# Optimization experiments

Hardware: AMD Instinct MI355X
Metric: run time of the kernel (lower is better)

Reference implementation:

```python
import jax, jax.numpy as jnp
import numpy as np

B, S, E, H = 4, 1024, 1024, 16
D = E // H          # head_dim = 64
ROT = 32            # rotary dims (first ROT channels of each head)


def _rope(x, freqs):
    # x: [B, H, S, D]; freqs: [1, 1, S, ROT]
    r = freqs.shape[-1]
    xl, xr = x[..., :r], x[..., r:]
    half = r // 2
    rot = jnp.concatenate([-xl[..., half:], xl[..., :half]], axis=-1)  # rotate_half
    xl = xl * jnp.cos(freqs) + rot * jnp.sin(freqs)
    return jnp.concatenate([xl, xr], axis=-1)


def setup_inputs() -> dict:
    key = jax.random.key(0)
    ks = jax.random.split(key, 7)
    std = 0.02
    return {
        "hidden_states": jax.random.normal(ks[0], (B, S, E), jnp.float32),
        "rotary_pos_emb": jax.random.normal(ks[1], (1, S, ROT), jnp.float32),
        "q_w": jax.random.normal(ks[2], (E, E), jnp.float32) * std,
        "k_w": jax.random.normal(ks[3], (E, E), jnp.float32) * std,
        "v_w": jax.random.normal(ks[4], (E, E), jnp.float32) * std,
        "o_w": jax.random.normal(ks[5], (E, E), jnp.float32) * std,
        "o_b": jnp.zeros((E,), jnp.float32),
    }


def reference(hidden_states, rotary_pos_emb, q_w, k_w, v_w, o_w, o_b):
    bsz, tgt_len, embed_dim = hidden_states.shape
    scale = D ** -0.5

    def shape(t):  # [B, S, E] -> [B, H, S, D]
        return t.reshape(bsz, tgt_len, H, D).transpose(0, 2, 1, 3)

    q = shape(hidden_states @ q_w.T * scale)
    k = shape(hidden_states @ k_w.T)
    v = shape(hidden_states @ v_w.T)

    freqs = rotary_pos_emb[:, None, :, :]  # [1, 1, S, ROT]
    q = _rope(q, freqs)
    k = _rope(k, freqs)
    v = _rope(v, freqs)

    attn = jnp.einsum("bhqd,bhkd->bhqk", q, k)
    causal = jnp.tril(jnp.ones((tgt_len, tgt_len), bool))
    attn = jnp.where(causal, attn, jnp.finfo(attn.dtype).min)
    attn = jax.nn.softmax(attn, axis=-1)

    out = jnp.einsum("bhqk,bhkd->bhqd", attn, v)
    out = out.transpose(0, 2, 1, 3).reshape(bsz, tgt_len, embed_dim)
    return out @ o_w.T + o_b
```

## Files before the change

kernel.cpp:

```cpp
#include <hip/hip_runtime.h>
#include <hip/hip_bf16.h>

typedef __bf16 bf16;
typedef __attribute__((ext_vector_type(2))) __bf16 bf16x2;
typedef __attribute__((ext_vector_type(4))) __bf16 bf16x4;
typedef __attribute__((ext_vector_type(8))) __bf16 bf16x8;
typedef __attribute__((ext_vector_type(4))) float f32x4;

#define NB 4
#define NS 1024
#define NE 1024
#define NH 16
#define ND 64
#define NROT 32
#define NM (NB*NS)

__device__ __forceinline__ void gload_lds16(const bf16* g, void* l) {
  __builtin_amdgcn_global_load_lds(
      (const __attribute__((address_space(1))) unsigned int*)g,
      (__attribute__((address_space(3))) unsigned int*)l,
      16, 0, 0);
}

template<int CTRL>
__device__ __forceinline__ float fmax_dpp(float x) {
  int y = __builtin_amdgcn_update_dpp(__float_as_int(x), __float_as_int(x),
                                      CTRL, 0xF, 0xF, false);
  return fmaxf(x, __int_as_float(y));
}
template<int CTRL>
__device__ __forceinline__ float fadd_dpp(float x) {
  int y = __builtin_amdgcn_update_dpp(__float_as_int(x), __float_as_int(x),
                                      CTRL, 0xF, 0xF, false);
  return x + __int_as_float(y);
}

__global__ void k_cvt(const float* __restrict__ src, bf16* __restrict__ dst, int n4) {
  int i = blockIdx.x * 256 + threadIdx.x;
  if (i >= n4) return;
  float4 v = reinterpret_cast<const float4*>(src)[i];
  bf16x4 o = { (bf16)v.x, (bf16)v.y, (bf16)v.z, (bf16)v.w };
  *reinterpret_cast<bf16x4*>(dst + (size_t)i * 4) = o;
}

struct Cvt4Args {
  const float* s0; const float* s1; const float* s2; const float* s3;
  bf16* d0; bf16* d1; bf16* d2; bf16* d3;
};
__global__ void k_cvt4(Cvt4Args a, int n4) {
  const float* s; bf16* d;
  switch (blockIdx.y) {
    case 0:  s = a.s0; d = a.d0; break;
    case 1:  s = a.s1; d = a.d1; break;
    case 2:  s = a.s2; d = a.d2; break;
    default: s = a.s3; d = a.d3; break;
  }
  int i = blockIdx.x * 256 + threadIdx.x;
  if (i >= n4) return;
  float4 v = reinterpret_cast<const float4*>(s)[i];
  bf16x4 o = { (bf16)v.x, (bf16)v.y, (bf16)v.z, (bf16)v.w };
  *reinterpret_cast<bf16x4*>(d + (size_t)i * 4) = o;
}

__global__ void k_tab(const float* __restrict__ rot, float* __restrict__ ct,
                      float* __restrict__ st, int n) {
  int i = blockIdx.x * 256 + threadIdx.x;
  if (i >= n) return;
  float v = rot[i];
  ct[i] = cosf(v);
  st[i] = sinf(v);
}

template<int BM, int BN, bool SWAP>
__device__ __forceinline__ void gemm_core(
    const bf16* __restrict__ A, const bf16* __restrict__ W,
    bf16* lA, bf16* lB, int m0, int n0, f32x4 (&acc)[BM/32][BN/32])
{
  const int tid = threadIdx.x;
  const int wave = tid >> 6, lane = tid & 63;
  const int wm = wave >> 1, wn = wave & 1;
  const int fr = lane & 15, kg = lane >> 4;
  const int lrow8 = lane >> 3, lslot = lane & 7;

  for (int kt = 0; kt < NE; kt += 64) {
#pragma unroll
    for (int i = 0; i < BM / 32; ++i) {
      int chunk = i * 4 + wave;
      int row = (chunk << 3) + lrow8;
      int slot = lslot ^ (row & 7);
      gload_lds16(A + (size_t)(m0 + row) * NE + kt + slot * 8, (char*)lA + chunk * 1024);
    }
#pragma unroll
    for (int i = 0; i < BN / 32; ++i) {
      int chunk = i * 4 + wave;
      int row = (chunk << 3) + lrow8;
      int slot = lslot ^ (row & 7);
      gload_lds16(W + (size_t)(n0 + row) * NE + kt + slot * 8, (char*)lB + chunk * 1024);
    }
    __syncthreads();
#pragma unroll
    for (int kk = 0; kk < 2; ++kk) {
      bf16x8 af[BM / 32], bfr[BN / 32];
#pragma unroll
      for (int i = 0; i < BM / 32; ++i) {
        int ra = wm * (BM / 2) + i * 16 + fr;
        af[i] = *reinterpret_cast<const bf16x8*>(lA + ra * 64 + (((kg + 4 * kk) ^ (ra & 7)) << 3));
      }
#pragma unroll
      for (int j = 0; j < BN / 32; ++j) {
        int rb = wn * (BN / 2) + j * 16 + fr;
        bfr[j] = *reinterpret_cast<const bf16x8*>(lB + rb * 64 + (((kg + 4 * kk) ^ (rb & 7)) << 3));
      }
#pragma unroll
      for (int i = 0; i < BM / 32; ++i)
#pragma unroll
        for (int j = 0; j < BN / 32; ++j) {
          if constexpr (SWAP)
            acc[j][i] = __builtin_amdgcn_mfma_f32_16x16x32_bf16(bfr[j], af[i], acc[j][i], 0, 0, 0);
          else
            acc[i][j] = __builtin_amdgcn_mfma_f32_16x16x32_bf16(af[i], bfr[j], acc[i][j], 0, 0, 0);
        }
    }
    __syncthreads();
  }
}

__global__ __launch_bounds__(256) void k_gemm_qk(
    const bf16* __restrict__ A, const bf16* __restrict__ Wq, const bf16* __restrict__ Wk,
    bf16* __restrict__ Oq, bf16* __restrict__ Ok,
    const float* __restrict__ ct, const float* __restrict__ st)
{
  __shared__ bf16 lA[128 * 64];
  __shared__ bf16 lB[128 * 64];
  const int z = blockIdx.z;
  const bf16* W = (z == 0) ? Wq : Wk;
  bf16* Og = (z == 0) ? Oq : Ok;
  const float scale = (z == 0) ? 0.125f * 1.44269504f : 1.0f;
  const int m0 = blockIdx.x * 128, n0 = blockIdx.y * 128;

  f32x4 acc[4][4] = {};
  gemm_core<128, 128, false>(A, W, lA, lB, m0, n0, acc);

  const int tid = threadIdx.x;
  const int wave = tid >> 6, lane = tid & 63;
  const int wm = wave >> 1, wn = wave & 1;
  const int fr = lane & 15, kg = lane >> 4;

#pragma unroll
  for (int i = 0; i < 4; ++i) {
    int rowbase = m0 + wm * 64 + i * 16 + kg * 4;
#pragma unroll
    for (int r = 0; r < 4; ++r) {
      int gm = rowbase + r;
      int s = gm & (NS - 1);
      float x0 = acc[i][0][r] * scale;
      float x1 = acc[i][1][r] * scale;
      float c0 = ct[s * NROT + fr],      sn0 = st[s * NROT + fr];
      float c1 = ct[s * NROT + 16 + fr], sn1 = st[s * NROT + 16 + fr];
      float y0 = x0 * c0 - x1 * sn0;
      float y1 = x1 * c1 + x0 * sn1;
      size_t rb = (size_t)gm * NE + n0 + wn * 64;
      Og[rb + 0 * 16 + fr] = (bf16)y0;
      Og[rb + 1 * 16 + fr] = (bf16)y1;
      Og[rb + 2 * 16 + fr] = (bf16)(acc[i][2][r] * scale);
      Og[rb + 3 * 16 + fr] = (bf16)(acc[i][3][r] * scale);
    }
  }
}

__global__ __launch_bounds__(256) void k_gemm_vt(
    const bf16* __restrict__ A, const bf16* __restrict__ W, bf16* __restrict__ vt,
    const float* __restrict__ ct, const float* __restrict__ st)
{
  __shared__ bf16 lA[128 * 64];
  __shared__ bf16 lB[128 * 64];
  const int m0 = blockIdx.x * 128, n0 = blockIdx.y * 128;
  f32x4 acc[4][4] = {};
  gemm_core<128, 128, true>(A, W, lA, lB, m0, n0, acc);

  const int tid = threadIdx.x;
  const int wave = tid >> 6, lane = tid & 63;
  const int wm = wave >> 1, wn = wave & 1;
  const int fr = lane & 15, kg = lane >> 4;
  const int b = m0 >> 10;
  const int h = (n0 + wn * 64) >> 6;
  bf16* vtb = vt + ((size_t)(b * 16 + h)) * ND * NS;

#pragma unroll
  for (int i = 0; i < 4; ++i) {
    int sl = (m0 & (NS - 1)) + wm * 64 + i * 16 + fr;
#pragma unroll
    for (int r = 0; r < 4; ++r) {
      int dbase = kg * 4 + r;
      float x0 = acc[0][i][r];
      float x1 = acc[1][i][r];
      float c0 = ct[sl * NROT + dbase],      sn0 = st[sl * NROT + dbase];
      float c1 = ct[sl * NROT + 16 + dbase], sn1 = st[sl * NROT + 16 + dbase];
      float y0 = x0 * c0 - x1 * sn0;
      float y1 = x1 * c1 + x0 * sn1;
      vtb[(size_t)(dbase)      * NS + sl] = (bf16)y0;
      vtb[(size_t)(16 + dbase) * NS + sl] = (bf16)y1;
      vtb[(size_t)(32 + dbase) * NS + sl] = (bf16)acc[2][i][r];
      vtb[(size_t)(48 + dbase) * NS + sl] = (bf16)acc[3][i][r];
    }
  }
}

__global__ __launch_bounds__(256) void k_gemm_o(
    const bf16* __restrict__ A, const bf16* __restrict__ W, float* __restrict__ Og,
    const float* __restrict__ bias)
{
  __shared__ bf16 lA[64 * 64];
  __shared__ bf16 lB[128 * 64];
  const int m0 = blockIdx.x * 64, n0 = blockIdx.y * 128;
  f32x4 acc[2][4] = {};
  gemm_core<64, 128, false>(A, W, lA, lB, m0, n0, acc);

  const int tid = threadIdx.x;
  const int wave = tid >> 6, lane = tid & 63;
  const int wm = wave >> 1, wn = wave & 1;
  const int fr = lane & 15, kg = lane >> 4;
#pragma unroll
  for (int i = 0; i < 2; ++i)
#pragma unroll
    for (int j = 0; j < 4; ++j) {
      int gc = n0 + wn * 64 + j * 16 + fr;
      float bv = bias[gc];
#pragma unroll
      for (int r = 0; r < 4; ++r) {
        int gm = m0 + wm * 32 + i * 16 + kg * 4 + r;
        Og[(size_t)gm * NE + gc] = acc[i][j][r] + bv;
      }
    }
}

__global__ __launch_bounds__(256) void k_attn(
    const bf16* __restrict__ Q, const bf16* __restrict__ K,
    const bf16* __restrict__ VT, bf16* __restrict__ O)
{
  __shared__ bf16 lK[2][64 * 64];
  __shared__ bf16 lVT[2][64 * 64];
  __shared__ bf16 lP[4][16 * 68];
  const int tid = threadIdx.x;
  const int wave = tid >> 6, lane = tid & 63;
  const int fr = lane & 15, kg = lane >> 4;

  const int p = blockIdx.y & 7;
  const int bh = blockIdx.x | ((blockIdx.y >> 3) << 3);
  const int b = bh >> 4, h = bh & 15;
  const int qtA = p, qtB = 15 - p;
  const int NT = 17;
  const bf16* Qb  = Q + (size_t)b * NS * NE + h * 64;
  const bf16* Kb  = K + (size_t)b * NS * NE + h * 64;
  const bf16* VTb = VT + (size_t)bh * ND * NS;
  bf16* Ob = O + (size_t)b * NS * NE + h * 64;

  bf16x8 qfA[2], qfB[2];
#pragma unroll
  for (int kk = 0; kk < 2; ++kk) {
    qfA[kk] = *reinterpret_cast<const bf16x8*>(
        Qb + (size_t)(qtA * 64 + wave * 16 + fr) * NE + kk * 32 + kg * 8);
    qfB[kk] = *reinterpret_cast<const bf16x8*>(
        Qb + (size_t)(qtB * 64 + wave * 16 + fr) * NE + kk * 32 + kg * 8);
  }

  auto stage = [&](int kv0, int buf) {
#pragma unroll
    for (int i = 0; i < 2; ++i) {
      int chunk = i * 4 + wave;
      int row = (chunk << 3) + (lane >> 3);
      int slot = (lane & 7) ^ (row & 7);
      gload_lds16(Kb + (size_t)(kv0 + row) * NE + slot * 8,
                  (char*)lK[buf] + chunk * 1024);
      gload_lds16(VTb + (size_t)row * NS + kv0 + slot * 8,
                  (char*)lVT[buf] + chunk * 1024);
    }
  };

  f32x4 oacc[4];
  float mrow[4], lsum[4];
  auto reset = [&]() {
#pragma unroll
    for (int r = 0; r < 4; ++r) {
      mrow[r] = -3.0e38f; lsum[r] = 0.f;
      oacc[r] = f32x4{0.f, 0.f, 0.f, 0.f};
    }
  };
  reset();

  auto epi = [&](int qt) {
#pragma unroll
    for (int df = 0; df < 4; ++df)
#pragma unroll
      for (int r = 0; r < 4; ++r)
        Ob[(size_t)(qt * 64 + wave * 16 + kg * 4 + r) * NE + df * 16 + fr] =
            (bf16)(oacc[df][r] / lsum[r]);
  };

  auto body = [&](const bf16x8 (&qf)[2], int c, bool diag) {
    const bf16* lKc  = lK[c];
    const bf16* lVTc = lVT[c];
    f32x4 sacc[4] = {};
    __builtin_amdgcn_s_setprio(1);
#pragma unroll
    for (int kk = 0; kk < 2; ++kk)
#pragma unroll
      for (int j = 0; j < 4; ++j) {
        int rc = j * 16 + fr;
        bf16x8 kf = *reinterpret_cast<const bf16x8*>(
            lKc + rc * 64 + (((kg + 4 * kk) ^ (rc & 7)) << 3));
        sacc[j] = __builtin_amdgcn_mfma_f32_16x16x32_bf16(qf[kk], kf, sacc[j], 0, 0, 0);
      }
    __builtin_amdgcn_s_setprio(0);

    if (diag) {
#pragma unroll
      for (int j = 0; j < 4; ++j)
#pragma unroll
        for (int r = 0; r < 4; ++r)
          if (j * 16 + fr > wave * 16 + kg * 4 + r) sacc[j][r] = -3.0e38f;
    }

    float tm[4]; float g = 0.f;
#pragma unroll
    for (int r = 0; r < 4; ++r) {
      float m4 = fmaxf(fmaxf(sacc[0][r], sacc[1][r]), fmaxf(sacc[2][r], sacc[3][r]));
      m4 = fmax_dpp<0x121>(m4); m4 = fmax_dpp<0x122>(m4);
      m4 = fmax_dpp<0x124>(m4); m4 = fmax_dpp<0x128>(m4);
      tm[r] = m4;
      g = fmaxf(g, m4 - mrow[r]);
    }
    if (!__all(g <= 8.0f)) {
#pragma unroll
      for (int r = 0; r < 4; ++r) {
        float nm = fmaxf(mrow[r], tm[r]);
        float corr = exp2f(mrow[r] - nm);
        mrow[r] = nm;
        lsum[r] *= corr;
#pragma unroll
        for (int df = 0; df < 4; ++df) oacc[df][r] *= corr;
      }
    }
#pragma unroll
    for (int r = 0; r < 4; ++r) {
      float ps = 0.f;
#pragma unroll
      for (int j = 0; j < 4; ++j) {
        float pv = exp2f(sacc[j][r] - mrow[r]);
        ps += pv;
        lP[wave][(kg * 4 + r) * 68 + j * 16 + fr] = (bf16)pv;
      }
      ps = fadd_dpp<0x121>(ps); ps = fadd_dpp<0x122>(ps);
      ps = fadd_dpp<0x124>(ps); ps = fadd_dpp<0x128>(ps);
      lsum[r] += ps;
    }

    __builtin_amdgcn_s_setprio(1);
#pragma unroll
    for (int ks = 0; ks < 2; ++ks) {
      bf16x8 pf = *reinterpret_cast<const bf16x8*>(&lP[wave][fr * 68 + ks * 32 + kg * 8]);
#pragma unroll
      for (int df = 0; df < 4; ++df) {
        int d = df * 16 + fr;
        bf16x8 vf = *reinterpret_cast<const bf16x8*>(
            lVTc + d * 64 + (((kg + 4 * ks) ^ (d & 7)) << 3));
        oacc[df] = __builtin_amdgcn_mfma_f32_16x16x32_bf16(pf, vf, oacc[df], 0, 0, 0);
      }
    }
    __builtin_amdgcn_s_setprio(0);
  };

  stage(0, 0);
  __syncthreads();

  for (int i = 0; i < NT; ++i) {
    const int c = i & 1;
    if (i + 1 < NT) {
      int i2 = i + 1;
      int t2 = (i2 > qtA) ? i2 - qtA - 1 : i2;
      stage(t2 * 64, c ^ 1);
    }
    if (i == qtA + 1) { epi(qtA); reset(); }
    if (i <= qtA) body(qfA, c, i == qtA);
    else          body(qfB, c, i == qtA + 1 + qtB);
    __syncthreads();
  }
  epi(qtB);
}

extern "C" void kernel_launch(void* const* d_in, const int* in_sizes, int n_in,
                              void* d_out, int out_size, void* d_ws, size_t ws_size,
                              hipStream_t stream) {
  const float* hs  = (const float*)d_in[0];
  const float* rot = (const float*)d_in[1];
  const float* qw  = (const float*)d_in[2];
  const float* kw  = (const float*)d_in[3];
  const float* vw  = (const float*)d_in[4];
  const float* ow  = (const float*)d_in[5];
  const float* obb = (const float*)d_in[6];
  float* out = (float*)d_out;

  char* ws = (char*)d_ws;
  size_t off = 0;
  bf16* hb  = (bf16*)(ws + off); off += (size_t)NM * NE * 2;
  bf16* wqb = (bf16*)(ws + off); off += (size_t)NE * NE * 2;
  bf16* wkb = (bf16*)(ws + off); off += (size_t)NE * NE * 2;
  bf16* wvb = (bf16*)(ws + off); off += (size_t)NE * NE * 2;
  bf16* wob = (bf16*)(ws + off); off += (size_t)NE * NE * 2;
  bf16* qb  = (bf16*)(ws + off); off += (size_t)NM * NE * 2;
  bf16* kb  = (bf16*)(ws + off); off += (size_t)NM * NE * 2;
  bf16* vt  = (bf16*)(ws + off); off += (size_t)NM * NE * 2;
  float* ct = (float*)(ws + off); off += (size_t)NS * NROT * 4;
  float* st = (float*)(ws + off); off += (size_t)NS * NROT * 4;
  bf16* aob = hb;

  k_cvt<<<dim3((NM * NE / 4 + 255) / 256), dim3(256), 0, stream>>>(hs, hb, NM * NE / 4);
  Cvt4Args ca = { qw, kw, vw, ow, wqb, wkb, wvb, wob };
  k_cvt4<<<dim3(NE * NE / 4 / 256, 4), dim3(256), 0, stream>>>(ca, NE * NE / 4);
  k_tab<<<dim3((NS * NROT + 255) / 256), dim3(256), 0, stream>>>(rot, ct, st, NS * NROT);

  k_gemm_qk<<<dim3(NM / 128, NE / 128, 2), dim3(256), 0, stream>>>(
      hb, wqb, wkb, qb, kb, ct, st);
  k_gemm_vt<<<dim3(NM / 128, NE / 128), dim3(256), 0, stream>>>(hb, wvb, vt, ct, st);

  k_attn<<<dim3(8, 64), dim3(256), 0, stream>>>(qb, kb, vt, aob);

  k_gemm_o<<<dim3(NM / 64, NE / 128), dim3(256), 0, stream>>>(aob, wob, out, obb);

  (void)in_sizes; (void)n_in; (void)out_size; (void)ws_size;
}
```

Measured before the change: 115.2 us.

## Split paired q-tile attention blocks into one q-tile per block with transposed S

The attention kernel drops the balanced pairing of two query tiles per block. It launches twice as many blocks, each handling one query tile, scheduled longest-first. The QK^T MFMA operands are swapped so each lane owns one query row, which turns the row max and row sum into shuffles across two lanes instead of DPP reductions. V is now single-buffered and loaded within the iteration, with an extra barrier before the K prefetch. This trades load balance and prefetch depth for more parallelism and cheaper softmax reductions.

```diff
diff --git a/kernel.cpp b/kernel.cpp
--- a/kernel.cpp
+++ b/kernel.cpp
@@ -20,19 +20,6 @@
       (const __attribute__((address_space(1))) unsigned int*)g,
       (__attribute__((address_space(3))) unsigned int*)l,
       16, 0, 0);
-}
-
-template<int CTRL>
-__device__ __forceinline__ float fmax_dpp(float x) {
-  int y = __builtin_amdgcn_update_dpp(__float_as_int(x), __float_as_int(x),
-                                      CTRL, 0xF, 0xF, false);
-  return fmaxf(x, __int_as_float(y));
-}
-template<int CTRL>
-__device__ __forceinline__ float fadd_dpp(float x) {
-  int y = __builtin_amdgcn_update_dpp(__float_as_int(x), __float_as_int(x),
-                                      CTRL, 0xF, 0xF, false);
-  return x + __int_as_float(y);
 }
 
 __global__ void k_cvt(const float* __restrict__ src, bf16* __restrict__ dst, int n4) {
@@ -239,67 +226,57 @@
     const bf16* __restrict__ VT, bf16* __restrict__ O)
 {
   __shared__ bf16 lK[2][64 * 64];
-  __shared__ bf16 lVT[2][64 * 64];
+  __shared__ bf16 lVT[64 * 64];
   __shared__ bf16 lP[4][16 * 68];
   const int tid = threadIdx.x;
   const int wave = tid >> 6, lane = tid & 63;
   const int fr = lane & 15, kg = lane >> 4;
 
-  const int p = blockIdx.y & 7;
-  const int bh = blockIdx.x | ((blockIdx.y >> 3) << 3);
+  const int qt = 15 - (blockIdx.y >> 3);
+  const int bh = blockIdx.x | ((blockIdx.y & 7) << 3);
   const int b = bh >> 4, h = bh & 15;
-  const int qtA = p, qtB = 15 - p;
-  const int NT = 17;
+  const int nt = qt + 1;
   const bf16* Qb  = Q + (size_t)b * NS * NE + h * 64;
   const bf16* Kb  = K + (size_t)b * NS * NE + h * 64;
   const bf16* VTb = VT + (size_t)bh * ND * NS;
   bf16* Ob = O + (size_t)b * NS * NE + h * 64;
 
-  bf16x8 qfA[2], qfB[2];
-#pragma unroll
-  for (int kk = 0; kk < 2; ++kk) {
-    qfA[kk] = *reinterpret_cast<const bf16x8*>(
-        Qb + (size_t)(qtA * 64 + wave * 16 + fr) * NE + kk * 32 + kg * 8);
-    qfB[kk] = *reinterpret_cast<const bf16x8*>(
-        Qb + (size_t)(qtB * 64 + wave * 16 + fr) * NE + kk * 32 + kg * 8);
-  }
-
-  auto stage = [&](int kv0, int buf) {
-#pragma unroll
-    for (int i = 0; i < 2; ++i) {
-      int chunk = i * 4 + wave;
-      int row = (chunk << 3) + (lane >> 3);
-      int slot = (lane & 7) ^ (row & 7);
-      gload_lds16(Kb + (size_t)(kv0 + row) * NE + slot * 8,
-                  (char*)lK[buf] + chunk * 1024);
-      gload_lds16(VTb + (size_t)row * NS + kv0 + slot * 8,
-                  (char*)lVT[buf] + chunk * 1024);
-    }
-  };
-
-  f32x4 oacc[4];
-  float mrow[4], lsum[4];
-  auto reset = [&]() {
-#pragma unroll
-    for (int r = 0; r < 4; ++r) {
-      mrow[r] = -3.0e38f; lsum[r] = 0.f;
-      oacc[r] = f32x4{0.f, 0.f, 0.f, 0.f};
-    }
-  };
-  reset();
-
-  auto epi = [&](int qt) {
-#pragma unroll
-    for (int df = 0; df < 4; ++df)
-#pragma unroll
-      for (int r = 0; r < 4; ++r)
-        Ob[(size_t)(qt * 64 + wave * 16 + kg * 4 + r) * NE + df * 16 + fr] =
-            (bf16)(oacc[df][r] / lsum[r]);
-  };
-
-  auto body = [&](const bf16x8 (&qf)[2], int c, bool diag) {
-    const bf16* lKc  = lK[c];
-    const bf16* lVTc = lVT[c];
+  const int qrow0 = qt * 64 + wave * 16;
+
+  bf16x8 qf[2];
+#pragma unroll
+  for (int kk = 0; kk < 2; ++kk)
+    qf[kk] = *reinterpret_cast<const bf16x8*>(
+        Qb + (size_t)(qrow0 + fr) * NE + kk * 32 + kg * 8);
+
+  const int srow = lane >> 3;
+  const int sslot = (lane & 7) ^ srow;
+  const int r0 = wave * 8 + srow;
+  const int r1 = (wave + 4) * 8 + srow;
+  const bf16* kA0 = Kb + (size_t)r0 * NE + sslot * 8;
+  const bf16* kA1 = Kb + (size_t)r1 * NE + sslot * 8;
+  const bf16* vA0 = VTb + (size_t)r0 * NS + sslot * 8;
+  const bf16* vA1 = VTb + (size_t)r1 * NS + sslot * 8;
+  char* ldsK0a = (char*)lK[0] + wave * 1024;
+  char* ldsK0b = (char*)lK[0] + (wave + 4) * 1024;
+  char* ldsK1a = (char*)lK[1] + wave * 1024;
+  char* ldsK1b = (char*)lK[1] + (wave + 4) * 1024;
+  char* ldsVa  = (char*)lVT + wave * 1024;
+  char* ldsVb  = (char*)lVT + (wave + 4) * 1024;
+
+  float m_ = -3.0e38f, l_ = 0.f;
+  f32x4 oacc[4] = {};
+
+  gload_lds16(kA0, ldsK0a);
+  gload_lds16(kA1, ldsK0b);
+  __syncthreads();
+
+  for (int t = 0; t < nt; ++t) {
+    const int c = t & 1;
+    gload_lds16(vA0 + t * 64, ldsVa);
+    gload_lds16(vA1 + t * 64, ldsVb);
+
+    const bf16* lKc = lK[c];
     f32x4 sacc[4] = {};
     __builtin_amdgcn_s_setprio(1);
 #pragma unroll
@@ -309,50 +286,61 @@
         int rc = j * 16 + fr;
         bf16x8 kf = *reinterpret_cast<const bf16x8*>(
             lKc + rc * 64 + (((kg + 4 * kk) ^ (rc & 7)) << 3));
-        sacc[j] = __builtin_amdgcn_mfma_f32_16x16x32_bf16(qf[kk], kf, sacc[j], 0, 0, 0);
+        sacc[j] = __builtin_amdgcn_mfma_f32_16x16x32_bf16(kf, qf[kk], sacc[j], 0, 0, 0);
       }
     __builtin_amdgcn_s_setprio(0);
 
-    if (diag) {
+    if (t == qt) {
+      const int ql = wave * 16 + fr;
 #pragma unroll
       for (int j = 0; j < 4; ++j)
 #pragma unroll
         for (int r = 0; r < 4; ++r)
-          if (j * 16 + fr > wave * 16 + kg * 4 + r) sacc[j][r] = -3.0e38f;
-    }
-
-    float tm[4]; float g = 0.f;
-#pragma unroll
-    for (int r = 0; r < 4; ++r) {
-      float m4 = fmaxf(fmaxf(sacc[0][r], sacc[1][r]), fmaxf(sacc[2][r], sacc[3][r]));
-      m4 = fmax_dpp<0x121>(m4); m4 = fmax_dpp<0x122>(m4);
-      m4 = fmax_dpp<0x124>(m4); m4 = fmax_dpp<0x128>(m4);
-      tm[r] = m4;
-      g = fmaxf(g, m4 - mrow[r]);
-    }
-    if (!__all(g <= 8.0f)) {
+          if (16 * j + 4 * kg + r > ql) sacc[j][r] = -3.0e38f;
+    }
+
+    float m4 = fmaxf(fmaxf(fmaxf(sacc[0][0], sacc[0][1]), fmaxf(sacc[0][2], sacc[0][3])),
+                     fmaxf(fmaxf(sacc[1][0], sacc[1][1]), fmaxf(sacc[1][2], sacc[1][3])));
+    m4 = fmaxf(m4, fmaxf(fmaxf(fmaxf(sacc[2][0], sacc[2][1]), fmaxf(sacc[2][2], sacc[2][3])),
+                         fmaxf(fmaxf(sacc[3][0], sacc[3][1]), fmaxf(sacc[3][2], sacc[3][3]))));
+    m4 = fmaxf(m4, __shfl_xor(m4, 16));
+    m4 = fmaxf(m4, __shfl_xor(m4, 32));
+
+    if (!__all(m4 - m_ <= 8.0f)) {
+      float nm = fmaxf(m_, m4);
+      float corr = exp2f(m_ - nm);
+      m_ = nm;
+      l_ *= corr;
 #pragma unroll
       for (int r = 0; r < 4; ++r) {
-        float nm = fmaxf(mrow[r], tm[r]);
-        float corr = exp2f(mrow[r] - nm);
-        mrow[r] = nm;
-        lsum[r] *= corr;
-#pragma unroll
-        for (int df = 0; df < 4; ++df) oacc[df][r] *= corr;
-      }
-    }
-#pragma unroll
-    for (int r = 0; r < 4; ++r) {
-      float ps = 0.f;
-#pragma unroll
-      for (int j = 0; j < 4; ++j) {
-        float pv = exp2f(sacc[j][r] - mrow[r]);
-        ps += pv;
-        lP[wave][(kg * 4 + r) * 68 + j * 16 + fr] = (bf16)pv;
-      }
-      ps = fadd_dpp<0x121>(ps); ps = fadd_dpp<0x122>(ps);
-      ps = fadd_dpp<0x124>(ps); ps = fadd_dpp<0x128>(ps);
-      lsum[r] += ps;
+        float cr = __shfl(corr, kg * 4 + r);
+#pragma unroll
+        for (int df = 0; df < 4; ++df) oacc[df][r] *= cr;
+      }
+    }
+
+    float ps = 0.f;
+#pragma unroll
+    for (int j = 0; j < 4; ++j) {
+      float p0 = exp2f(sacc[j][0] - m_);
+      float p1 = exp2f(sacc[j][1] - m_);
+      float p2 = exp2f(sacc[j][2] - m_);
+      float p3 = exp2f(sacc[j][3] - m_);
+      ps += (p0 + p1) + (p2 + p3);
+      bf16x4 pp = { (bf16)p0, (bf16)p1, (bf16)p2, (bf16)p3 };
+      *reinterpret_cast<bf16x4*>(&lP[wave][fr * 68 + j * 16 + kg * 4]) = pp;
+    }
+    ps += __shfl_xor(ps, 16);
+    ps += __shfl_xor(ps, 32);
+    l_ += ps;
+
+    __syncthreads();
+
+    if (t + 1 < nt) {
+      const bf16* ka = kA0 + (size_t)(t + 1) * 64 * NE;
+      const bf16* kb2 = kA1 + (size_t)(t + 1) * 64 * NE;
+      if (c) { gload_lds16(ka, ldsK0a); gload_lds16(kb2, ldsK0b); }
+      else   { gload_lds16(ka, ldsK1a); gload_lds16(kb2, ldsK1b); }
     }
 
     __builtin_amdgcn_s_setprio(1);
@@ -363,29 +351,23 @@
       for (int df = 0; df < 4; ++df) {
         int d = df * 16 + fr;
         bf16x8 vf = *reinterpret_cast<const bf16x8*>(
-            lVTc + d * 64 + (((kg + 4 * ks) ^ (d & 7)) << 3));
+            (const bf16*)lVT + d * 64 + (((kg + 4 * ks) ^ (d & 7)) << 3));
         oacc[df] = __builtin_amdgcn_mfma_f32_16x16x32_bf16(pf, vf, oacc[df], 0, 0, 0);
       }
     }
     __builtin_amdgcn_s_setprio(0);
-  };
-
-  stage(0, 0);
-  __syncthreads();
-
-  for (int i = 0; i < NT; ++i) {
-    const int c = i & 1;
-    if (i + 1 < NT) {
-      int i2 = i + 1;
-      int t2 = (i2 > qtA) ? i2 - qtA - 1 : i2;
-      stage(t2 * 64, c ^ 1);
-    }
-    if (i == qtA + 1) { epi(qtA); reset(); }
-    if (i <= qtA) body(qfA, c, i == qtA);
-    else          body(qfB, c, i == qtA + 1 + qtB);
+
     __syncthreads();
   }
-  epi(qtB);
+
+  float linv[4];
+#pragma unroll
+  for (int r = 0; r < 4; ++r) linv[r] = 1.0f / __shfl(l_, kg * 4 + r);
+#pragma unroll
+  for (int df = 0; df < 4; ++df)
+#pragma unroll
+    for (int r = 0; r < 4; ++r)
+      Ob[(size_t)(qrow0 + kg * 4 + r) * NE + df * 16 + fr] = (bf16)(oacc[df][r] * linv[r]);
 }
 
 extern "C" void kernel_launch(void* const* d_in, const int* in_sizes, int n_in,
@@ -423,7 +405,7 @@
       hb, wqb, wkb, qb, kb, ct, st);
   k_gemm_vt<<<dim3(NM / 128, NE / 128), dim3(256), 0, stream>>>(hb, wvb, vt, ct, st);
 
-  k_attn<<<dim3(8, 64), dim3(256), 0, stream>>>(qb, kb, vt, aob);
+  k_attn<<<dim3(8, 128), dim3(256), 0, stream>>>(qb, kb, vt, aob);
 
   k_gemm_o<<<dim3(NM / 64, NE / 128), dim3(256), 0, stream>>>(aob, wob, out, obb);
 
```

Result: faster. 104.4 us (-9.4%).
